# Kernel tuning notes

Hardware: AMD Instinct MI355X
Metric: run time of the kernel (lower is better)

## Reference

```python
import jax, jax.numpy as jnp
import numpy as np

IN_FEATURES = 4096
OUT_FEATURES = 768
N_BITS = 8
SCALE = float(2 ** N_BITS - 1)  # 255
REG_WEIGHT = 0.001


def setup_inputs() -> dict:
    key = jax.random.key(0)
    k1, k2, k3 = jax.random.split(key, 3)
    latent = jax.random.normal(k1, (1024, IN_FEATURES), dtype=jnp.float32)
    true_sum = jax.random.uniform(k2, (1024, OUT_FEATURES * N_BITS), dtype=jnp.float32)
    # nn.init.uniform_(weight, -0.1, 0.1)
    weight = jax.random.uniform(k3, (IN_FEATURES, OUT_FEATURES * N_BITS),
                                dtype=jnp.float32, minval=-0.1, maxval=0.1)
    return {"latent": latent, "true_sum": true_sum, "weight": weight}


def _powers():
    # [1, 2, 4, ..., 2^(n-1)] with the top (sign) bit negated -> two's complement
    p = 2.0 ** jnp.arange(N_BITS, dtype=jnp.float32)
    return p.at[-1].multiply(-1.0)


def reference(latent, true_sum, weight):
    prob_weights = jax.nn.sigmoid(weight)                      # [in, out*n_bits]
    # min(|p-0|, |p-1|) = min(p, 1-p) for p in (0,1)
    reg_loss = REG_WEIGHT * jnp.minimum(prob_weights, 1.0 - prob_weights).mean()

    powers = _powers()                                         # [n_bits]
    int_weights = jnp.einsum('iob,b->io',
                             prob_weights.reshape(IN_FEATURES, -1, N_BITS),
                             powers)                           # [in, out]
    int_sum = jnp.einsum('nob,b->no',
                         true_sum.reshape(true_sum.shape[0], -1, N_BITS),
                         powers)                               # [B, out]

    # (latent[:, :, None] * int_weights[None]).sum(-2) == latent @ int_weights
    pred = jnp.einsum('bi,io->bo', latent, int_weights)        # [B, out]

    recon_loss = jnp.mean((pred / SCALE - int_sum / SCALE) ** 2)
    return (recon_loss + reg_loss, recon_loss, reg_loss)
```

## Files before the change

kernel.cpp:

```cpp
#include <hip/hip_runtime.h>
#include <hip/hip_bf16.h>
#include <stdint.h>

#define IN_F   4096
#define OUT_F  768
#define OUTB   (OUT_F * 8)
#define BATCH  1024
#define SPLITK 4
#define KSPAN  (IN_F / SPLITK)
#define NIT    (KSPAN / 32)

typedef short short8  __attribute__((ext_vector_type(8)));
typedef float f32x4   __attribute__((ext_vector_type(4)));
typedef unsigned int u32;

__device__ __forceinline__ ushort f2bf(float f) {
    uint32_t u = __builtin_bit_cast(uint32_t, f);
    u += 0x7FFFu + ((u >> 16) & 1u);
    return (ushort)(u >> 16);
}

__device__ __forceinline__ float waveReduceSum(float v) {
    #pragma unroll
    for (int off = 32; off > 0; off >>= 1) v += __shfl_down(v, off, 64);
    return v;
}

__device__ __forceinline__ void glds16(const void* g, void* l) {
    __builtin_amdgcn_global_load_lds(
        (const __attribute__((address_space(1))) u32*)g,
        (__attribute__((address_space(3))) u32*)l, 16, 0, 0);
}

#define WS_PRED  256
#define WS_WP    (WS_PRED + 3145728)
#define WS_LABF  (WS_WP + 6291456)

__global__ __launch_bounds__(256) void k_prep(const float* __restrict__ latent,
                                              float* __restrict__ accum,
                                              float* __restrict__ pred,
                                              ushort* __restrict__ labf) {
    int i = blockIdx.x * 256 + threadIdx.x;
    if (i == 0) { accum[0] = 0.f; accum[1] = 0.f; }
    if (i < (BATCH * OUT_F) / 4) ((float4*)pred)[i] = make_float4(0.f, 0.f, 0.f, 0.f);
    float4 a0 = ((const float4*)latent)[2 * i];
    float4 a1 = ((const float4*)latent)[2 * i + 1];
    union { ushort u[8]; uint4 v; } pk;
    pk.u[0] = f2bf(a0.x); pk.u[1] = f2bf(a0.y); pk.u[2] = f2bf(a0.z); pk.u[3] = f2bf(a0.w);
    pk.u[4] = f2bf(a1.x); pk.u[5] = f2bf(a1.y); pk.u[6] = f2bf(a1.z); pk.u[7] = f2bf(a1.w);
    ((uint4*)labf)[i] = pk.v;
}

__global__ __launch_bounds__(256) void k_weights(const float* __restrict__ w,
                                                 ushort* __restrict__ wp,
                                                 float* __restrict__ accum) {
    int t  = blockIdx.x * 256 + threadIdx.x;
    int o  = t % OUT_F;
    int i8 = t / OUT_F;
    const float* src = w + (size_t)(i8 * 8) * OUTB + (size_t)o * 8;

    const float P[8] = {1.f, 2.f, 4.f, 8.f, 16.f, 32.f, 64.f, -128.f};
    float regsum = 0.f;
    union { ushort u[8]; uint4 v; } pk;

    #pragma unroll
    for (int r = 0; r < 8; r++) {
        float4 a = *(const float4*)(src + (size_t)r * OUTB);
        float4 b = *(const float4*)(src + (size_t)r * OUTB + 4);
        float x[8] = {a.x, a.y, a.z, a.w, b.x, b.y, b.z, b.w};
        float iw = 0.f;
        #pragma unroll
        for (int j = 0; j < 8; j++) {
            float p = __builtin_amdgcn_rcpf(1.f + __expf(-x[j]));
            iw += p * P[j];
            regsum += fminf(p, 1.f - p);
        }
        pk.u[r] = f2bf(iw);
    }
    *(uint4*)(wp + ((size_t)i8 * OUT_F + o) * 8) = pk.v;

    float ws = waveReduceSum(regsum);
    __shared__ float red[4];
    int lane = threadIdx.x & 63, wv = threadIdx.x >> 6;
    if (lane == 0) red[wv] = ws;
    __syncthreads();
    if (threadIdx.x == 0) atomicAdd(accum + 1, red[0] + red[1] + red[2] + red[3]);
}

__global__ __launch_bounds__(256) void k_gemm(const ushort* __restrict__ labf,
                                              const ushort* __restrict__ wp,
                                              float* __restrict__ pred) {
    __shared__ __align__(16) ushort lA[2][64 * 40];
    __shared__ __align__(16) ushort lB[2][4 * 1032];

    const int tid  = threadIdx.x;
    const int n0   = blockIdx.x * 64;
    const int m0   = blockIdx.y * 64;
    const int kbase = blockIdx.z * KSPAN;
    const int lane = tid & 63, w = tid >> 6;
    const int wm = w >> 1, wn = w & 1;
    const int quad = lane >> 4, l16 = lane & 15;

    f32x4 acc[2][2] = {{{0.f,0.f,0.f,0.f},{0.f,0.f,0.f,0.f}},
                       {{0.f,0.f,0.f,0.f},{0.f,0.f,0.f,0.f}}};

    const int ar = tid >> 2, ac = tid & 3;
    const ushort* aptr = labf + (size_t)(m0 + ar) * IN_F + kbase + ac * 8;
    const ushort* bptr = wp + ((size_t)(kbase / 8 + w) * OUT_F + n0 + lane) * 8;

    int buf = 0;
    glds16(bptr, &lB[0][w * 1032]);
    uint4 aR = *(const uint4*)aptr;
    *(uint4*)&lA[0][ar * 40 + ac * 8] = aR;
    __syncthreads();

    for (int it = 0; it < NIT; ++it) {
        const int nxt = buf ^ 1;
        if (it + 1 < NIT) {
            glds16(bptr + (size_t)(it + 1) * 4 * OUT_F * 8, &lB[nxt][w * 1032]);
            aR = *(const uint4*)(aptr + (it + 1) * 32);
        }
        short8 af0 = *(short8*)&lA[buf][(wm * 32 + l16) * 40 + quad * 8];
        short8 af1 = *(short8*)&lA[buf][(wm * 32 + 16 + l16) * 40 + quad * 8];
        short8 bf0 = *(short8*)&lB[buf][quad * 1032 + (wn * 32 + l16) * 8];
        short8 bf1 = *(short8*)&lB[buf][quad * 1032 + (wn * 32 + 16 + l16) * 8];
        acc[0][0] = __builtin_amdgcn_mfma_f32_16x16x32_bf16(af0, bf0, acc[0][0], 0, 0, 0);
        acc[0][1] = __builtin_amdgcn_mfma_f32_16x16x32_bf16(af0, bf1, acc[0][1], 0, 0, 0);
        acc[1][0] = __builtin_amdgcn_mfma_f32_16x16x32_bf16(af1, bf0, acc[1][0], 0, 0, 0);
        acc[1][1] = __builtin_amdgcn_mfma_f32_16x16x32_bf16(af1, bf1, acc[1][1], 0, 0, 0);
        if (it + 1 < NIT) *(uint4*)&lA[nxt][ar * 40 + ac * 8] = aR;
        __syncthreads();
        buf = nxt;
    }

    #pragma unroll
    for (int fm = 0; fm < 2; fm++)
    #pragma unroll
    for (int fn = 0; fn < 2; fn++)
    #pragma unroll
    for (int r = 0; r < 4; r++) {
        int m = m0 + wm * 32 + fm * 16 + quad * 4 + r;
        int n = n0 + wn * 32 + fn * 16 + l16;
        atomicAdd(&pred[(size_t)m * OUT_F + n], acc[fm][fn][r]);
    }
}

__global__ __launch_bounds__(256) void k_epi(const float* __restrict__ pred,
                                             const float* __restrict__ tsum,
                                             float* __restrict__ accum) {
    int i = blockIdx.x * 256 + threadIdx.x;
    int m = i / (OUT_F / 4);
    int c = i % (OUT_F / 4);
    float4 p = ((const float4*)pred)[(size_t)m * (OUT_F / 4) + c];
    const float* ts = tsum + (size_t)m * OUTB + (size_t)c * 32;
    float lsum = 0.f;
    float pv[4] = {p.x, p.y, p.z, p.w};
    #pragma unroll
    for (int j = 0; j < 4; j++) {
        float4 t0 = *(const float4*)(ts + j * 8);
        float4 t1 = *(const float4*)(ts + j * 8 + 4);
        float isum = t0.x + 2.f * t0.y + 4.f * t0.z + 8.f * t0.w
                   + 16.f * t1.x + 32.f * t1.y + 64.f * t1.z - 128.f * t1.w;
        float d = pv[j] - isum;
        lsum += d * d;
    }
    float wsum = waveReduceSum(lsum);
    __shared__ float red[4];
    if ((threadIdx.x & 63) == 0) red[threadIdx.x >> 6] = wsum;
    __syncthreads();
    if (threadIdx.x == 0) atomicAdd(accum + 0, red[0] + red[1] + red[2] + red[3]);
}

__global__ void k_fin(const float* __restrict__ accum, float* __restrict__ out) {
    float recon = accum[0] / ((float)(BATCH * OUT_F) * 255.f * 255.f);
    float reg   = 0.001f * accum[1] / (float)((size_t)IN_F * OUTB);
    out[0] = recon + reg;
    out[1] = recon;
    out[2] = reg;
}

extern "C" void kernel_launch(void* const* d_in, const int* in_sizes, int n_in,
                              void* d_out, int out_size, void* d_ws, size_t ws_size,
                              hipStream_t stream) {
    const float* latent = (const float*)d_in[0];
    const float* tsum   = (const float*)d_in[1];
    const float* weight = (const float*)d_in[2];
    float* out   = (float*)d_out;
    float* accum = (float*)d_ws;
    float* pred  = (float*)((char*)d_ws + WS_PRED);
    ushort* wp   = (ushort*)((char*)d_ws + WS_WP);
    ushort* labf = (ushort*)((char*)d_ws + WS_LABF);

    k_prep<<<2048, 256, 0, stream>>>(latent, accum, pred, labf);
    k_weights<<<(512 * OUT_F) / 256, 256, 0, stream>>>(weight, wp, accum);
    k_gemm<<<dim3(OUT_F / 64, BATCH / 64, SPLITK), 256, 0, stream>>>(labf, wp, pred);
    k_epi<<<(BATCH * OUT_F / 4) / 256, 256, 0, stream>>>(pred, tsum, accum);
    k_fin<<<1, 1, 0, stream>>>(accum, out);
}
```

Before: 221.2 us.

## Merge prep into weight kernel and replace split-K atomics with partial planes

Folds the latent bf16 conversion into the weight-quantization kernel as extra blocks, which removes one launch and the zeroing of pred. The split-K GEMM now stores each K-slice into its own fp32 plane instead of doing global atomicAdds, and the epilogue sums the four planes. The global reduction atomics are replaced by per-block partial sums that a 256-thread final kernel reduces. The cost is extra workspace and extra traffic for writing and reading four prediction planes.

```diff
diff --git a/kernel.cpp b/kernel.cpp
--- a/kernel.cpp
+++ b/kernel.cpp
@@ -9,6 +9,7 @@
 #define SPLITK 4
 #define KSPAN  (IN_F / SPLITK)
 #define NIT    (KSPAN / 32)
+#define PLANE  (BATCH * OUT_F)
 
 typedef short short8  __attribute__((ext_vector_type(8)));
 typedef float f32x4   __attribute__((ext_vector_type(4)));
@@ -32,28 +33,33 @@
         (__attribute__((address_space(3))) u32*)l, 16, 0, 0);
 }
 
-#define WS_PRED  256
-#define WS_WP    (WS_PRED + 3145728)
-#define WS_LABF  (WS_WP + 6291456)
-
-__global__ __launch_bounds__(256) void k_prep(const float* __restrict__ latent,
-                                              float* __restrict__ accum,
-                                              float* __restrict__ pred,
-                                              ushort* __restrict__ labf) {
-    int i = blockIdx.x * 256 + threadIdx.x;
-    if (i == 0) { accum[0] = 0.f; accum[1] = 0.f; }
-    if (i < (BATCH * OUT_F) / 4) ((float4*)pred)[i] = make_float4(0.f, 0.f, 0.f, 0.f);
-    float4 a0 = ((const float4*)latent)[2 * i];
-    float4 a1 = ((const float4*)latent)[2 * i + 1];
-    union { ushort u[8]; uint4 v; } pk;
-    pk.u[0] = f2bf(a0.x); pk.u[1] = f2bf(a0.y); pk.u[2] = f2bf(a0.z); pk.u[3] = f2bf(a0.w);
-    pk.u[4] = f2bf(a1.x); pk.u[5] = f2bf(a1.y); pk.u[6] = f2bf(a1.z); pk.u[7] = f2bf(a1.w);
-    ((uint4*)labf)[i] = pk.v;
-}
+#define WS_WP    12582912
+#define WS_LABF  18874368
+#define WS_REGP  27262976
+#define WS_SQP   27269120
 
 __global__ __launch_bounds__(256) void k_weights(const float* __restrict__ w,
+                                                 const float* __restrict__ latent,
                                                  ushort* __restrict__ wp,
-                                                 float* __restrict__ accum) {
+                                                 ushort* __restrict__ labf,
+                                                 float* __restrict__ regpart) {
+    if (blockIdx.x >= 1536) {
+        int t = (blockIdx.x - 1536) * 256 + threadIdx.x;
+        const float4* src = (const float4*)latent;
+        uint4* dst = (uint4*)labf;
+        #pragma unroll
+        for (int j = 0; j < 4; j++) {
+            int o = j * 131072 + t;
+            float4 a0 = src[2 * o];
+            float4 a1 = src[2 * o + 1];
+            union { ushort u[8]; uint4 v; } pk;
+            pk.u[0] = f2bf(a0.x); pk.u[1] = f2bf(a0.y); pk.u[2] = f2bf(a0.z); pk.u[3] = f2bf(a0.w);
+            pk.u[4] = f2bf(a1.x); pk.u[5] = f2bf(a1.y); pk.u[6] = f2bf(a1.z); pk.u[7] = f2bf(a1.w);
+            dst[o] = pk.v;
+        }
+        return;
+    }
+
     int t  = blockIdx.x * 256 + threadIdx.x;
     int o  = t % OUT_F;
     int i8 = t / OUT_F;
@@ -84,12 +90,12 @@
     int lane = threadIdx.x & 63, wv = threadIdx.x >> 6;
     if (lane == 0) red[wv] = ws;
     __syncthreads();
-    if (threadIdx.x == 0) atomicAdd(accum + 1, red[0] + red[1] + red[2] + red[3]);
+    if (threadIdx.x == 0) regpart[blockIdx.x] = red[0] + red[1] + red[2] + red[3];
 }
 
 __global__ __launch_bounds__(256) void k_gemm(const ushort* __restrict__ labf,
                                               const ushort* __restrict__ wp,
-                                              float* __restrict__ pred) {
+                                              float* __restrict__ predp) {
     __shared__ __align__(16) ushort lA[2][64 * 40];
     __shared__ __align__(16) ushort lB[2][4 * 1032];
 
@@ -133,6 +139,7 @@
         buf = nxt;
     }
 
+    float* plane = predp + (size_t)blockIdx.z * PLANE;
     #pragma unroll
     for (int fm = 0; fm < 2; fm++)
     #pragma unroll
@@ -141,42 +148,57 @@
     for (int r = 0; r < 4; r++) {
         int m = m0 + wm * 32 + fm * 16 + quad * 4 + r;
         int n = n0 + wn * 32 + fn * 16 + l16;
-        atomicAdd(&pred[(size_t)m * OUT_F + n], acc[fm][fn][r]);
-    }
-}
-
-__global__ __launch_bounds__(256) void k_epi(const float* __restrict__ pred,
+        plane[(size_t)m * OUT_F + n] = acc[fm][fn][r];
+    }
+}
+
+__global__ __launch_bounds__(256) void k_epi(const float* __restrict__ predp,
                                              const float* __restrict__ tsum,
-                                             float* __restrict__ accum) {
-    int i = blockIdx.x * 256 + threadIdx.x;
-    int m = i / (OUT_F / 4);
-    int c = i % (OUT_F / 4);
-    float4 p = ((const float4*)pred)[(size_t)m * (OUT_F / 4) + c];
-    const float* ts = tsum + (size_t)m * OUTB + (size_t)c * 32;
-    float lsum = 0.f;
-    float pv[4] = {p.x, p.y, p.z, p.w};
-    #pragma unroll
-    for (int j = 0; j < 4; j++) {
-        float4 t0 = *(const float4*)(ts + j * 8);
-        float4 t1 = *(const float4*)(ts + j * 8 + 4);
-        float isum = t0.x + 2.f * t0.y + 4.f * t0.z + 8.f * t0.w
-                   + 16.f * t1.x + 32.f * t1.y + 64.f * t1.z - 128.f * t1.w;
-        float d = pv[j] - isum;
-        lsum += d * d;
-    }
+                                             float* __restrict__ sqpart) {
+    int n = blockIdx.x * 256 + threadIdx.x;
+    int m = blockIdx.y;
+    size_t idx = (size_t)m * OUT_F + n;
+    float p = predp[idx] + predp[idx + PLANE] + predp[idx + 2 * PLANE] + predp[idx + 3 * PLANE];
+    const float* ts = tsum + (size_t)m * OUTB + (size_t)n * 8;
+    float4 t0 = *(const float4*)ts;
+    float4 t1 = *(const float4*)(ts + 4);
+    float isum = t0.x + 2.f * t0.y + 4.f * t0.z + 8.f * t0.w
+               + 16.f * t1.x + 32.f * t1.y + 64.f * t1.z - 128.f * t1.w;
+    float d = p - isum;
+    float lsum = d * d;
+
     float wsum = waveReduceSum(lsum);
     __shared__ float red[4];
     if ((threadIdx.x & 63) == 0) red[threadIdx.x >> 6] = wsum;
     __syncthreads();
-    if (threadIdx.x == 0) atomicAdd(accum + 0, red[0] + red[1] + red[2] + red[3]);
-}
-
-__global__ void k_fin(const float* __restrict__ accum, float* __restrict__ out) {
-    float recon = accum[0] / ((float)(BATCH * OUT_F) * 255.f * 255.f);
-    float reg   = 0.001f * accum[1] / (float)((size_t)IN_F * OUTB);
-    out[0] = recon + reg;
-    out[1] = recon;
-    out[2] = reg;
+    if (threadIdx.x == 0)
+        sqpart[blockIdx.y * 3 + blockIdx.x] = red[0] + red[1] + red[2] + red[3];
+}
+
+__global__ __launch_bounds__(256) void k_fin(const float* __restrict__ regpart,
+                                             const float* __restrict__ sqpart,
+                                             float* __restrict__ out) {
+    int tid = threadIdx.x;
+    float r = 0.f, s = 0.f;
+    #pragma unroll
+    for (int j = 0; j < 6; j++) r += regpart[tid + j * 256];
+    #pragma unroll
+    for (int j = 0; j < 12; j++) s += sqpart[tid + j * 256];
+    r = waveReduceSum(r);
+    s = waveReduceSum(s);
+    __shared__ float redR[4], redS[4];
+    int lane = tid & 63, wv = tid >> 6;
+    if (lane == 0) { redR[wv] = r; redS[wv] = s; }
+    __syncthreads();
+    if (tid == 0) {
+        float R = redR[0] + redR[1] + redR[2] + redR[3];
+        float S = redS[0] + redS[1] + redS[2] + redS[3];
+        float recon = S / ((float)(BATCH * OUT_F) * 255.f * 255.f);
+        float reg   = 0.001f * R / (float)((size_t)IN_F * OUTB);
+        out[0] = recon + reg;
+        out[1] = recon;
+        out[2] = reg;
+    }
 }
 
 extern "C" void kernel_launch(void* const* d_in, const int* in_sizes, int n_in,
@@ -185,15 +207,15 @@
     const float* latent = (const float*)d_in[0];
     const float* tsum   = (const float*)d_in[1];
     const float* weight = (const float*)d_in[2];
-    float* out   = (float*)d_out;
-    float* accum = (float*)d_ws;
-    float* pred  = (float*)((char*)d_ws + WS_PRED);
-    ushort* wp   = (ushort*)((char*)d_ws + WS_WP);
-    ushort* labf = (ushort*)((char*)d_ws + WS_LABF);
-
-    k_prep<<<2048, 256, 0, stream>>>(latent, accum, pred, labf);
-    k_weights<<<(512 * OUT_F) / 256, 256, 0, stream>>>(weight, wp, accum);
-    k_gemm<<<dim3(OUT_F / 64, BATCH / 64, SPLITK), 256, 0, stream>>>(labf, wp, pred);
-    k_epi<<<(BATCH * OUT_F / 4) / 256, 256, 0, stream>>>(pred, tsum, accum);
-    k_fin<<<1, 1, 0, stream>>>(accum, out);
-}
+    float* out     = (float*)d_out;
+    float* predp   = (float*)d_ws;
+    ushort* wp     = (ushort*)((char*)d_ws + WS_WP);
+    ushort* labf   = (ushort*)((char*)d_ws + WS_LABF);
+    float* regpart = (float*)((char*)d_ws + WS_REGP);
+    float* sqpart  = (float*)((char*)d_ws + WS_SQP);
+
+    k_weights<<<2048, 256, 0, stream>>>(weight, latent, wp, labf, regpart);
+    k_gemm<<<dim3(OUT_F / 64, BATCH / 64, SPLITK), 256, 0, stream>>>(labf, wp, predp);
+    k_epi<<<dim3(3, BATCH), 256, 0, stream>>>(predp, tsum, sqpart);
+    k_fin<<<1, 256, 0, stream>>>(regpart, sqpart, out);
+}
```

Result: faster. 204.5 us (-7.5%).
